# Optimization experiments

Hardware: AMD Instinct MI355X
Metric: run time of the kernel (lower is better)

## Reference

```python
import jax, jax.numpy as jnp
import numpy as np

N = 10            # n_wires
DIM = 1 << N      # 1024 state dimension
HID = 64          # number of Pauli-string observables
B, T = 4, 512

_CNOT = jnp.array([[1, 0, 0, 0], [0, 1, 0, 0], [0, 0, 0, 1], [0, 0, 1, 0]], dtype=jnp.complex64)
# 0:I 1:X 2:Y 3:Z
_PAULIS = jnp.array([[[1, 0], [0, 1]],
                     [[0, 1], [1, 0]],
                     [[0, -1j], [1j, 0]],
                     [[1, 0], [0, -1]]], dtype=jnp.complex64)

def _rx(t):
    c = jnp.cos(t / 2).astype(jnp.complex64)
    s = jnp.sin(t / 2).astype(jnp.complex64)
    return jnp.stack([jnp.stack([c, -1j * s]), jnp.stack([-1j * s, c])])

def _ry(t):
    c = jnp.cos(t / 2).astype(jnp.complex64)
    s = jnp.sin(t / 2).astype(jnp.complex64)
    return jnp.stack([jnp.stack([c, -s]), jnp.stack([s, c])])

def _apply(U, gate, qubits):
    # U <- expand_operator(gate, qubits, N) @ U, without materializing the expansion.
    # Row index bits: qubit 0 is the most significant bit (matches expand_operator).
    m = len(qubits)
    Tn = U.reshape((2,) * N + (DIM,))
    Tn = jnp.moveaxis(Tn, qubits, tuple(range(m)))
    Tn = (gate @ Tn.reshape(1 << m, -1)).reshape((2,) * N + (DIM,))
    Tn = jnp.moveaxis(Tn, tuple(range(m)), qubits)
    return Tn.reshape(DIM, DIM)

def _build_U(rx0, ry0, ry1):
    U = jnp.eye(DIM, dtype=jnp.complex64)
    for j in range(N):
        U = _apply(U, _rx(rx0[j]), (j,))
        U = _apply(U, _ry(ry0[j]), (j,))
    for j in range(N):
        U = _apply(U, _CNOT, (j, (j + 1) % N))  # control j, target (j+1)%N
    for j in range(N):
        U = _apply(U, _ry(ry1[j]), (j,))
    return U

def _build_obs(op_codes):
    # O[h] = kron of Paulis along the wire axis (qubit 0 leftmost / most significant).
    mats = _PAULIS[op_codes]  # (H, N, 2, 2)
    O = jnp.ones((op_codes.shape[0], 1, 1), jnp.complex64)
    for q in range(N):
        d = O.shape[-1]
        O = jnp.einsum('hij,hkl->hikjl', O, mats[:, q]).reshape(-1, 2 * d, 2 * d)
    return O  # (H, DIM, DIM)

def setup_inputs() -> dict:
    key = jax.random.key(0)
    ks = jax.random.split(key, 5)
    pi = 3.14159265
    return {
        'x': jax.random.normal(ks[0], (B, T, DIM), jnp.float32),
        'rx0': jax.random.uniform(ks[1], (N,), jnp.float32, -pi, pi),
        'ry0': jax.random.uniform(ks[2], (N,), jnp.float32, -pi, pi),
        'ry1': jax.random.uniform(ks[3], (N,), jnp.float32, -pi, pi),
        'op_codes': jax.random.randint(ks[4], (HID, N), 0, 4),
    }

def reference(x, rx0, ry0, ry1, op_codes):
    U = _build_U(rx0, ry0, ry1)
    O = _build_obs(op_codes)
    b, t, c = x.shape
    xf = x.reshape(b * t, c)
    # AmplitudeEncoder: L2-normalize each row into a complex state vector.
    psi = (xf / jnp.linalg.norm(xf, axis=-1, keepdims=True)).astype(jnp.complex64)
    # <psi| U^dag O U |psi> = <phi| O |phi> with phi = U psi  (same math as obs_primes)
    phi = psi @ U.T  # (BT, DIM)
    exps = jnp.einsum('bd,odk,bk->bo', phi.conj(), O, phi).real
    return exps.reshape(b, t, -1).astype(jnp.float32)
```

## Files before the change

kernel.cpp:

```cpp
#include <hip/hip_runtime.h>
#include <math.h>

#define NQ 10
#define DIM 1024
#define HID 64
#define NT 256

template<int CTRL>
__device__ __forceinline__ float fdpp(float v) {
    return __int_as_float(__builtin_amdgcn_update_dpp(
        0, __float_as_int(v), CTRL, 0xF, 0xF, true));
}

__device__ __forceinline__ void l1pair(float4 g, float& r0, float& i0, float& r1, float& i1) {
    float n0r = g.x * r0 - g.y * i0 - g.z * r1 + g.w * i1;
    float n0i = g.x * i0 + g.y * r0 - g.z * i1 - g.w * r1;
    float n1r = g.z * r0 + g.w * i0 + g.x * r1 + g.y * i1;
    float n1i = g.z * i0 - g.w * r0 + g.x * i1 - g.y * r1;
    r0 = n0r; i0 = n0i; r1 = n1r; i1 = n1i;
}
__device__ __forceinline__ void l2pair(float2 g, float& r0, float& i0, float& r1, float& i1) {
    float n0r = g.x * r0 - g.y * r1, n0i = g.x * i0 - g.y * i1;
    float n1r = g.y * r0 + g.x * r1, n1i = g.y * i0 + g.x * i1;
    r0 = n0r; i0 = n0i; r1 = n1r; i1 = n1i;
}

template<int P>
__device__ __forceinline__ float xl(float v) {
    if constexpr (P == 0)      return fdpp<0xB1>(v);
    else if constexpr (P == 1) return fdpp<0x4E>(v);
    else                       return __shfl_xor(v, 1 << P, 64);
}

template<int P>
__device__ __forceinline__ void gate4_l1(float4 g, int tid, float (&vr)[4], float (&vi)[4]) {
    const float fsb = ((tid >> P) & 1) ? 1.f : -1.f;
    const float Bs = fsb * g.y, Cs = fsb * g.z;
    #pragma unroll
    for (int m = 0; m < 4; m++) {
        float ur = xl<P>(vr[m]);
        float ui = xl<P>(vi[m]);
        float nr = g.x * vr[m] + Bs * vi[m] + Cs * ur + g.w * ui;
        float ni = g.x * vi[m] - Bs * vr[m] + Cs * ui - g.w * ur;
        vr[m] = nr; vi[m] = ni;
    }
}
template<int P>
__device__ __forceinline__ void gate4_l2(float2 g, int tid, float (&vr)[4], float (&vi)[4]) {
    const float fsb = ((tid >> P) & 1) ? 1.f : -1.f;
    const float ssf = fsb * g.y;
    #pragma unroll
    for (int m = 0; m < 4; m++) {
        float ur = xl<P>(vr[m]);
        float ui = xl<P>(vi[m]);
        vr[m] = g.x * vr[m] + ssf * ur;
        vi[m] = g.x * vi[m] + ssf * ui;
    }
}

template<int PASS, int HB, int CM>
__device__ __forceinline__ float obs_halved_p(const float (&vr)[8], const float (&vi)[8],
                                              const char* stb, int base_cx, int w1) {
    float a0 = 0.f, a1 = 0.f;
    if constexpr (HB == 3) {
        if constexpr (PASS == 1) return 0.f;
        #pragma unroll
        for (int j = 0; j < 8; j++) {
            const int r = j;
            const float2 c = *(const float2*)(stb + (base_cx ^ (r << 9)));
            float t;
            if constexpr (CM) t = vr[j] * c.y - vi[j] * c.x;
            else              t = vr[j] * c.x + vi[j] * c.y;
            const int cf = 0x40000000 | (((w1 >> r) & 1) << 31);
            if (j & 1) a1 = fmaf(__int_as_float(cf), t, a1);
            else       a0 = fmaf(__int_as_float(cf), t, a0);
        }
    } else {
        #pragma unroll
        for (int ii = 0; ii < 4; ii++) {
            const int idx = PASS * 4 + ii;
            const int r   = ((idx >> HB) << (HB + 1)) | (idx & ((1 << HB) - 1));
            const int j   = r - PASS * 8;
            const float2 c = *(const float2*)(stb + (base_cx ^ (r << 9)));
            float t;
            if constexpr (CM) t = vr[j] * c.y - vi[j] * c.x;
            else              t = vr[j] * c.x + vi[j] * c.y;
            const int cf = 0x40000000 | (((w1 >> r) & 1) << 31);
            if (ii & 1) a1 = fmaf(__int_as_float(cf), t, a1);
            else        a0 = fmaf(__int_as_float(cf), t, a0);
        }
    }
    return a0 + a1;
}
template<int PASS, int CM>
__device__ __forceinline__ float obs_full_p(const float (&vr)[8], const float (&vi)[8],
                                            const char* stb, int base_c, int w1) {
    float a0 = 0.f, a1 = 0.f;
    #pragma unroll
    for (int j = 0; j < 8; j++) {
        const int r = PASS * 8 + j;
        const float2 c = *(const float2*)(stb + base_c + (r << 9));
        float t;
        if constexpr (CM) t = vr[j] * c.y - vi[j] * c.x;
        else              t = vr[j] * c.x + vi[j] * c.y;
        const int cf = 0x3F800000 | (((w1 >> r) & 1) << 31);
        if (j & 1) a1 = fmaf(__int_as_float(cf), t, a1);
        else       a0 = fmaf(__int_as_float(cf), t, a0);
    }
    return a0 + a1;
}
template<int PASS>
__device__ __forceinline__ float obs_diag_p(const float (&vr)[8], const float (&vi)[8], int w1) {
    float a0 = 0.f, a1 = 0.f;
    #pragma unroll
    for (int j = 0; j < 8; j++) {
        const int r = PASS * 8 + j;
        float t = fmaf(vr[j], vr[j], vi[j] * vi[j]);
        const int cf = 0x3F800000 | (((w1 >> r) & 1) << 31);
        if (j & 1) a1 = fmaf(__int_as_float(cf), t, a1);
        else       a0 = fmaf(__int_as_float(cf), t, a0);
    }
    return a0 + a1;
}
__device__ __forceinline__ int4 make_meta(const int* op_codes, int o) {
    int xm = 0, yzm = 0, ny = 0;
    #pragma unroll
    for (int q = 0; q < NQ; q++) {
        int code = op_codes[o * NQ + q];
        int bit  = 1 << (NQ - 1 - q);
        if (code == 1) xm |= bit;
        else if (code == 2) { xm |= bit; yzm |= bit; ny++; }
        else if (code == 3) yzm |= bit;
    }
    const int cm = ny & 1, gflip = (ny >> 1) & 1;
    const int yh = yzm >> 6;
    int w1 = 0;
    #pragma unroll
    for (int r = 0; r < 16; r++)
        w1 |= ((__popc(r & yh) & 1) ^ gflip) << r;
    const int xmr = (xm >> 6) & 15;
    int hbc;
    if (xm == 0)      hbc = 5;
    else if (xmr)     hbc = __ffs(xmr) - 1;
    else              hbc = 4;
    return make_int4(xm, yzm & 63, w1, hbc | (cm << 3));
}
template<int PASS>
__device__ __forceinline__ float obs_one_p(int4 mt, int lane,
        const float (&vr)[8], const float (&vi)[8], const char* stb) {
    const int xm   = __builtin_amdgcn_readfirstlane(mt.x);
    const int yzml = __builtin_amdgcn_readfirstlane(mt.y);
    const int w1   = __builtin_amdgcn_readfirstlane(mt.z);
    const int knd  = __builtin_amdgcn_readfirstlane(mt.w);
    const int hbc = knd & 7, cm = knd >> 3;
    float p;
    if (hbc == 5) {
        p = obs_diag_p<PASS>(vr, vi, w1);
    } else {
        const int xml = xm & 63, xmr = (xm >> 6) & 15;
        const int base_cx = (xmr << 9) | ((lane ^ xml) << 3);
        switch (hbc | (cm << 3)) {
            case 0:     p = obs_halved_p<PASS,0,0>(vr, vi, stb, base_cx, w1); break;
            case 1:     p = obs_halved_p<PASS,1,0>(vr, vi, stb, base_cx, w1); break;
            case 2:     p = obs_halved_p<PASS,2,0>(vr, vi, stb, base_cx, w1); break;
            case 3:     p = obs_halved_p<PASS,3,0>(vr, vi, stb, base_cx, w1); break;
            case 4:     p = obs_full_p<PASS,0>(vr, vi, stb, base_cx, w1);     break;
            case 8 | 0: p = obs_halved_p<PASS,0,1>(vr, vi, stb, base_cx, w1); break;
            case 8 | 1: p = obs_halved_p<PASS,1,1>(vr, vi, stb, base_cx, w1); break;
            case 8 | 2: p = obs_halved_p<PASS,2,1>(vr, vi, stb, base_cx, w1); break;
            case 8 | 3: p = obs_halved_p<PASS,3,1>(vr, vi, stb, base_cx, w1); break;
            default:    p = obs_full_p<PASS,1>(vr, vi, stb, base_cx, w1);     break;
        }
    }
    const int sl = __popc(lane & yzml) & 1;
    return __int_as_float(__float_as_int(p) ^ (sl << 31));
}

__global__ __launch_bounds__(NT, 6) void qsa_kernel(
    const float* __restrict__ x,
    const float* __restrict__ rx0,
    const float* __restrict__ ry0,
    const float* __restrict__ ry1,
    const int*   __restrict__ op_codes,
    float* __restrict__ out)
{
    __shared__ float2 st[DIM];
    __shared__ float  cb[4][64 * 17];
    __shared__ float4 s_l1[NQ];
    __shared__ float2 s_l2[NQ];
    __shared__ int4   s_meta[HID];
    __shared__ float  wsum[4];

    const int tid  = threadIdx.x;
    const int lane = tid & 63;
    const int wave = tid >> 6;
    const int row  = blockIdx.x;

    if (tid < NQ) {
        float a = 0.5f * rx0[tid], b = 0.5f * ry0[tid];
        float c1 = cosf(a), s1 = sinf(a), c2 = cosf(b), s2 = sinf(b);
        s_l1[tid] = make_float4(c1 * c2, s1 * s2, s2 * c1, c2 * s1);
    } else if (tid < 2 * NQ) {
        float a = 0.5f * ry1[tid - NQ];
        s_l2[tid - NQ] = make_float2(cosf(a), sinf(a));
    }
    if (tid >= 64 && tid < 64 + HID)
        s_meta[tid - 64] = make_meta(op_codes, tid - 64);

    float vr[4], vi[4];
    float ssq = 0.f;
    const float* xr = x + (size_t)row * DIM;
    #pragma unroll
    for (int m = 0; m < 4; m++) {
        vr[m] = xr[tid + NT * m];
        vi[m] = 0.f;
        ssq += vr[m] * vr[m];
    }
    #pragma unroll
    for (int off = 32; off; off >>= 1) ssq += __shfl_xor(ssq, off, 64);
    if (lane == 0) wsum[wave] = ssq;
    __syncthreads();
    {
        float inv = 1.0f / sqrtf(wsum[0] + wsum[1] + wsum[2] + wsum[3]);
        #pragma unroll
        for (int m = 0; m < 4; m++) vr[m] *= inv;
    }

    {
        float4 g0 = s_l1[0];
        l1pair(g0, vr[0], vi[0], vr[2], vi[2]);
        l1pair(g0, vr[1], vi[1], vr[3], vi[3]);
        float4 g1 = s_l1[1];
        l1pair(g1, vr[0], vi[0], vr[1], vi[1]);
        l1pair(g1, vr[2], vi[2], vr[3], vi[3]);
    }
    #pragma unroll
    for (int m = 0; m < 4; m++) st[tid + NT * m] = make_float2(vr[m], vi[m]);
    __syncthreads();
    {
        int base = lane | (wave << 8);
        float2 w00 = st[base], w01 = st[base | 64], w10 = st[base | 128], w11 = st[base | 192];
        float4 g2 = s_l1[2], g3 = s_l1[3];
        l1pair(g2, w00.x, w00.y, w10.x, w10.y);
        l1pair(g2, w01.x, w01.y, w11.x, w11.y);
        l1pair(g3, w00.x, w00.y, w01.x, w01.y);
        l1pair(g3, w10.x, w10.y, w11.x, w11.y);
        st[base] = w00; st[base | 64] = w01; st[base | 128] = w10; st[base | 192] = w11;
    }
    __syncthreads();
    #pragma unroll
    for (int m = 0; m < 4; m++) { float2 t = st[tid + NT * m]; vr[m] = t.x; vi[m] = t.y; }
    gate4_l1<5>(s_l1[4], tid, vr, vi);
    gate4_l1<4>(s_l1[5], tid, vr, vi);
    gate4_l1<3>(s_l1[6], tid, vr, vi);
    gate4_l1<2>(s_l1[7], tid, vr, vi);
    gate4_l1<1>(s_l1[8], tid, vr, vi);
    gate4_l1<0>(s_l1[9], tid, vr, vi);

    #pragma unroll
    for (int m = 0; m < 4; m++) st[tid + NT * m] = make_float2(vr[m], vi[m]);
    __syncthreads();
    #pragma unroll
    for (int m = 0; m < 4; m++) {
        int d = tid + NT * m;
        int src = (d ^ (d >> 1)) ^ ((d & 1) * 0x300);
        float2 t = st[src];
        vr[m] = t.x; vi[m] = t.y;
    }
    __syncthreads();

    {
        float2 g0 = s_l2[0];
        l2pair(g0, vr[0], vi[0], vr[2], vi[2]);
        l2pair(g0, vr[1], vi[1], vr[3], vi[3]);
        float2 g1 = s_l2[1];
        l2pair(g1, vr[0], vi[0], vr[1], vi[1]);
        l2pair(g1, vr[2], vi[2], vr[3], vi[3]);
    }
    #pragma unroll
    for (int m = 0; m < 4; m++) st[tid + NT * m] = make_float2(vr[m], vi[m]);
    __syncthreads();
    {
        int base = lane | (wave << 8);
        float2 w00 = st[base], w01 = st[base | 64], w10 = st[base | 128], w11 = st[base | 192];
        float2 g2 = s_l2[2], g3 = s_l2[3];
        l2pair(g2, w00.x, w00.y, w10.x, w10.y);
        l2pair(g2, w01.x, w01.y, w11.x, w11.y);
        l2pair(g3, w00.x, w00.y, w01.x, w01.y);
        l2pair(g3, w10.x, w10.y, w11.x, w11.y);
        st[base] = w00; st[base | 64] = w01; st[base | 128] = w10; st[base | 192] = w11;
    }
    __syncthreads();
    #pragma unroll
    for (int m = 0; m < 4; m++) { float2 t = st[tid + NT * m]; vr[m] = t.x; vi[m] = t.y; }
    gate4_l2<5>(s_l2[4], tid, vr, vi);
    gate4_l2<4>(s_l2[5], tid, vr, vi);
    gate4_l2<3>(s_l2[6], tid, vr, vi);
    gate4_l2<2>(s_l2[7], tid, vr, vi);
    gate4_l2<1>(s_l2[8], tid, vr, vi);
    gate4_l2<0>(s_l2[9], tid, vr, vi);
    #pragma unroll
    for (int m = 0; m < 4; m++) st[tid + NT * m] = make_float2(vr[m], vi[m]);
    __syncthreads();

    const char* stb = (const char*)st;
    float* cbw = &cb[wave][lane * 17];
    const float* cbr = &cb[wave][(lane >> 4) * (16 * 17) + (lane & 15)];
    {
        float vra[8], via[8];
        #pragma unroll
        for (int j = 0; j < 8; j++) {
            float2 t = st[(j << 6) | lane];
            vra[j] = t.x; via[j] = t.y;
        }
        #pragma unroll 2
        for (int oo = 0; oo < 16; oo++)
            cbw[oo] = obs_one_p<0>(s_meta[(wave << 4) + oo], lane, vra, via, stb);
        #pragma unroll
        for (int j = 0; j < 8; j++) {
            float2 t = st[((8 + j) << 6) | lane];
            vra[j] = t.x; via[j] = t.y;
        }
        #pragma unroll 2
        for (int oo = 0; oo < 16; oo++)
            cbw[oo] += obs_one_p<1>(s_meta[(wave << 4) + oo], lane, vra, via, stb);
    }
    float s0 = 0.f, s1 = 0.f, s2 = 0.f, s3 = 0.f;
    #pragma unroll
    for (int k = 0; k < 16; k += 4) {
        s0 += cbr[(k + 0) * 17];
        s1 += cbr[(k + 1) * 17];
        s2 += cbr[(k + 2) * 17];
        s3 += cbr[(k + 3) * 17];
    }
    float tot = (s0 + s1) + (s2 + s3);
    tot += __shfl_xor(tot, 16, 64);
    tot += __shfl_xor(tot, 32, 64);
    if (lane < 16)
        out[(size_t)row * HID + (wave << 4) + lane] = tot;
}

extern "C" void kernel_launch(void* const* d_in, const int* in_sizes, int n_in,
                              void* d_out, int out_size, void* d_ws, size_t ws_size,
                              hipStream_t stream) {
    const float* x   = (const float*)d_in[0];
    const float* rx0 = (const float*)d_in[1];
    const float* ry0 = (const float*)d_in[2];
    const float* ry1 = (const float*)d_in[3];
    const int*   op  = (const int*)d_in[4];
    float* o = (float*)d_out;
    const int rows = in_sizes[0] / DIM;
    qsa_kernel<<<rows, NT, 0, stream>>>(x, rx0, ry0, ry1, op, o);
}
```

Before: 39.11 us.

## Process two state rows per block, sharing gate and observable metadata

Each block now simulates two input rows together, storing their complex amplitudes interleaved as float4 in shared memory. Gate coefficients, observable metadata, branch decisions and the shared-memory coefficient reads are amortized across both rows. The observable reduction is split into two chunks of eight to bound register use, and launch bounds drop from 6 to 4 waves per SIMD. The cost is higher register and LDS pressure, and half as many blocks, which lowers occupancy and parallelism.

New measurement: 70.41 us. 80.0% more time.

```diff
diff --git a/kernel.cpp b/kernel.cpp
--- a/kernel.cpp
+++ b/kernel.cpp
@@ -59,21 +59,23 @@
 }
 
 template<int PASS, int HB, int CM>
-__device__ __forceinline__ float obs_halved_p(const float (&vr)[8], const float (&vi)[8],
-                                              const char* stb, int base_cx, int w1) {
-    float a0 = 0.f, a1 = 0.f;
+__device__ __forceinline__ float2 obs_halved_p2(
+        const float (&a0r)[8], const float (&a0i)[8],
+        const float (&a1r)[8], const float (&a1i)[8],
+        const char* stb, int base_cx, int w1) {
+    float p0 = 0.f, p1 = 0.f;
     if constexpr (HB == 3) {
-        if constexpr (PASS == 1) return 0.f;
+        if constexpr (PASS == 1) return make_float2(0.f, 0.f);
         #pragma unroll
         for (int j = 0; j < 8; j++) {
-            const int r = j;
-            const float2 c = *(const float2*)(stb + (base_cx ^ (r << 9)));
-            float t;
-            if constexpr (CM) t = vr[j] * c.y - vi[j] * c.x;
-            else              t = vr[j] * c.x + vi[j] * c.y;
-            const int cf = 0x40000000 | (((w1 >> r) & 1) << 31);
-            if (j & 1) a1 = fmaf(__int_as_float(cf), t, a1);
-            else       a0 = fmaf(__int_as_float(cf), t, a0);
+            const float4 c = *(const float4*)(stb + (base_cx ^ (j << 10)));
+            float t0, t1;
+            if constexpr (CM) { t0 = a0r[j] * c.y - a0i[j] * c.x;
+                                t1 = a1r[j] * c.w - a1i[j] * c.z; }
+            else              { t0 = a0r[j] * c.x + a0i[j] * c.y;
+                                t1 = a1r[j] * c.z + a1i[j] * c.w; }
+            const float cf = __int_as_float(0x40000000 | (((w1 >> j) & 1) << 31));
+            p0 = fmaf(cf, t0, p0); p1 = fmaf(cf, t1, p1);
         }
     } else {
         #pragma unroll
@@ -81,46 +83,52 @@
             const int idx = PASS * 4 + ii;
             const int r   = ((idx >> HB) << (HB + 1)) | (idx & ((1 << HB) - 1));
             const int j   = r - PASS * 8;
-            const float2 c = *(const float2*)(stb + (base_cx ^ (r << 9)));
-            float t;
-            if constexpr (CM) t = vr[j] * c.y - vi[j] * c.x;
-            else              t = vr[j] * c.x + vi[j] * c.y;
-            const int cf = 0x40000000 | (((w1 >> r) & 1) << 31);
-            if (ii & 1) a1 = fmaf(__int_as_float(cf), t, a1);
-            else        a0 = fmaf(__int_as_float(cf), t, a0);
-        }
-    }
-    return a0 + a1;
+            const float4 c = *(const float4*)(stb + (base_cx ^ (r << 10)));
+            float t0, t1;
+            if constexpr (CM) { t0 = a0r[j] * c.y - a0i[j] * c.x;
+                                t1 = a1r[j] * c.w - a1i[j] * c.z; }
+            else              { t0 = a0r[j] * c.x + a0i[j] * c.y;
+                                t1 = a1r[j] * c.z + a1i[j] * c.w; }
+            const float cf = __int_as_float(0x40000000 | (((w1 >> r) & 1) << 31));
+            p0 = fmaf(cf, t0, p0); p1 = fmaf(cf, t1, p1);
+        }
+    }
+    return make_float2(p0, p1);
 }
 template<int PASS, int CM>
-__device__ __forceinline__ float obs_full_p(const float (&vr)[8], const float (&vi)[8],
-                                            const char* stb, int base_c, int w1) {
-    float a0 = 0.f, a1 = 0.f;
+__device__ __forceinline__ float2 obs_full_p2(
+        const float (&a0r)[8], const float (&a0i)[8],
+        const float (&a1r)[8], const float (&a1i)[8],
+        const char* stb, int base_c, int w1) {
+    float p0 = 0.f, p1 = 0.f;
     #pragma unroll
     for (int j = 0; j < 8; j++) {
         const int r = PASS * 8 + j;
-        const float2 c = *(const float2*)(stb + base_c + (r << 9));
-        float t;
-        if constexpr (CM) t = vr[j] * c.y - vi[j] * c.x;
-        else              t = vr[j] * c.x + vi[j] * c.y;
-        const int cf = 0x3F800000 | (((w1 >> r) & 1) << 31);
-        if (j & 1) a1 = fmaf(__int_as_float(cf), t, a1);
-        else       a0 = fmaf(__int_as_float(cf), t, a0);
-    }
-    return a0 + a1;
+        const float4 c = *(const float4*)(stb + (base_c ^ (r << 10)));
+        float t0, t1;
+        if constexpr (CM) { t0 = a0r[j] * c.y - a0i[j] * c.x;
+                            t1 = a1r[j] * c.w - a1i[j] * c.z; }
+        else              { t0 = a0r[j] * c.x + a0i[j] * c.y;
+                            t1 = a1r[j] * c.z + a1i[j] * c.w; }
+        const float cf = __int_as_float(0x3F800000 | (((w1 >> r) & 1) << 31));
+        p0 = fmaf(cf, t0, p0); p1 = fmaf(cf, t1, p1);
+    }
+    return make_float2(p0, p1);
 }
 template<int PASS>
-__device__ __forceinline__ float obs_diag_p(const float (&vr)[8], const float (&vi)[8], int w1) {
-    float a0 = 0.f, a1 = 0.f;
+__device__ __forceinline__ float2 obs_diag_p2(
+        const float (&a0r)[8], const float (&a0i)[8],
+        const float (&a1r)[8], const float (&a1i)[8], int w1) {
+    float p0 = 0.f, p1 = 0.f;
     #pragma unroll
     for (int j = 0; j < 8; j++) {
         const int r = PASS * 8 + j;
-        float t = fmaf(vr[j], vr[j], vi[j] * vi[j]);
-        const int cf = 0x3F800000 | (((w1 >> r) & 1) << 31);
-        if (j & 1) a1 = fmaf(__int_as_float(cf), t, a1);
-        else       a0 = fmaf(__int_as_float(cf), t, a0);
-    }
-    return a0 + a1;
+        float t0 = fmaf(a0r[j], a0r[j], a0i[j] * a0i[j]);
+        float t1 = fmaf(a1r[j], a1r[j], a1i[j] * a1i[j]);
+        const float cf = __int_as_float(0x3F800000 | (((w1 >> r) & 1) << 31));
+        p0 = fmaf(cf, t0, p0); p1 = fmaf(cf, t1, p1);
+    }
+    return make_float2(p0, p1);
 }
 __device__ __forceinline__ int4 make_meta(const int* op_codes, int o) {
     int xm = 0, yzm = 0, ny = 0;
@@ -146,37 +154,40 @@
     return make_int4(xm, yzm & 63, w1, hbc | (cm << 3));
 }
 template<int PASS>
-__device__ __forceinline__ float obs_one_p(int4 mt, int lane,
-        const float (&vr)[8], const float (&vi)[8], const char* stb) {
+__device__ __forceinline__ float2 obs_one_p2(int4 mt, int lane,
+        const float (&a0r)[8], const float (&a0i)[8],
+        const float (&a1r)[8], const float (&a1i)[8], const char* stb) {
     const int xm   = __builtin_amdgcn_readfirstlane(mt.x);
     const int yzml = __builtin_amdgcn_readfirstlane(mt.y);
     const int w1   = __builtin_amdgcn_readfirstlane(mt.z);
     const int knd  = __builtin_amdgcn_readfirstlane(mt.w);
     const int hbc = knd & 7, cm = knd >> 3;
-    float p;
+    float2 p;
     if (hbc == 5) {
-        p = obs_diag_p<PASS>(vr, vi, w1);
+        p = obs_diag_p2<PASS>(a0r, a0i, a1r, a1i, w1);
     } else {
         const int xml = xm & 63, xmr = (xm >> 6) & 15;
-        const int base_cx = (xmr << 9) | ((lane ^ xml) << 3);
+        const int base_cx = (xmr << 10) | ((lane ^ xml) << 4);
         switch (hbc | (cm << 3)) {
-            case 0:     p = obs_halved_p<PASS,0,0>(vr, vi, stb, base_cx, w1); break;
-            case 1:     p = obs_halved_p<PASS,1,0>(vr, vi, stb, base_cx, w1); break;
-            case 2:     p = obs_halved_p<PASS,2,0>(vr, vi, stb, base_cx, w1); break;
-            case 3:     p = obs_halved_p<PASS,3,0>(vr, vi, stb, base_cx, w1); break;
-            case 4:     p = obs_full_p<PASS,0>(vr, vi, stb, base_cx, w1);     break;
-            case 8 | 0: p = obs_halved_p<PASS,0,1>(vr, vi, stb, base_cx, w1); break;
-            case 8 | 1: p = obs_halved_p<PASS,1,1>(vr, vi, stb, base_cx, w1); break;
-            case 8 | 2: p = obs_halved_p<PASS,2,1>(vr, vi, stb, base_cx, w1); break;
-            case 8 | 3: p = obs_halved_p<PASS,3,1>(vr, vi, stb, base_cx, w1); break;
-            default:    p = obs_full_p<PASS,1>(vr, vi, stb, base_cx, w1);     break;
-        }
-    }
-    const int sl = __popc(lane & yzml) & 1;
-    return __int_as_float(__float_as_int(p) ^ (sl << 31));
-}
-
-__global__ __launch_bounds__(NT, 6) void qsa_kernel(
+            case 0:     p = obs_halved_p2<PASS,0,0>(a0r,a0i,a1r,a1i, stb, base_cx, w1); break;
+            case 1:     p = obs_halved_p2<PASS,1,0>(a0r,a0i,a1r,a1i, stb, base_cx, w1); break;
+            case 2:     p = obs_halved_p2<PASS,2,0>(a0r,a0i,a1r,a1i, stb, base_cx, w1); break;
+            case 3:     p = obs_halved_p2<PASS,3,0>(a0r,a0i,a1r,a1i, stb, base_cx, w1); break;
+            case 4:     p = obs_full_p2<PASS,0>(a0r,a0i,a1r,a1i, stb, base_cx, w1);     break;
+            case 8 | 0: p = obs_halved_p2<PASS,0,1>(a0r,a0i,a1r,a1i, stb, base_cx, w1); break;
+            case 8 | 1: p = obs_halved_p2<PASS,1,1>(a0r,a0i,a1r,a1i, stb, base_cx, w1); break;
+            case 8 | 2: p = obs_halved_p2<PASS,2,1>(a0r,a0i,a1r,a1i, stb, base_cx, w1); break;
+            case 8 | 3: p = obs_halved_p2<PASS,3,1>(a0r,a0i,a1r,a1i, stb, base_cx, w1); break;
+            default:    p = obs_full_p2<PASS,1>(a0r,a0i,a1r,a1i, stb, base_cx, w1);     break;
+        }
+    }
+    const int slb = (__popc(lane & yzml) & 1) << 31;
+    p.x = __int_as_float(__float_as_int(p.x) ^ slb);
+    p.y = __int_as_float(__float_as_int(p.y) ^ slb);
+    return p;
+}
+
+__global__ __launch_bounds__(NT, 4) void qsa_kernel(
     const float* __restrict__ x,
     const float* __restrict__ rx0,
     const float* __restrict__ ry0,
@@ -184,17 +195,18 @@
     const int*   __restrict__ op_codes,
     float* __restrict__ out)
 {
-    __shared__ float2 st[DIM];
-    __shared__ float  cb[4][64 * 17];
+    __shared__ float4 st4[DIM];
+    __shared__ float2 cb[4][64 * 9];
     __shared__ float4 s_l1[NQ];
     __shared__ float2 s_l2[NQ];
     __shared__ int4   s_meta[HID];
-    __shared__ float  wsum[4];
+    __shared__ float2 wsum[4];
 
     const int tid  = threadIdx.x;
     const int lane = tid & 63;
     const int wave = tid >> 6;
-    const int row  = blockIdx.x;
+    const int row0 = blockIdx.x * 2;
+    const int row1 = row0 + 1;
 
     if (tid < NQ) {
         float a = 0.5f * rx0[tid], b = 0.5f * ry0[tid];
@@ -207,137 +219,164 @@
     if (tid >= 64 && tid < 64 + HID)
         s_meta[tid - 64] = make_meta(op_codes, tid - 64);
 
-    float vr[4], vi[4];
-    float ssq = 0.f;
-    const float* xr = x + (size_t)row * DIM;
-    #pragma unroll
-    for (int m = 0; m < 4; m++) {
-        vr[m] = xr[tid + NT * m];
-        vi[m] = 0.f;
-        ssq += vr[m] * vr[m];
-    }
-    #pragma unroll
-    for (int off = 32; off; off >>= 1) ssq += __shfl_xor(ssq, off, 64);
-    if (lane == 0) wsum[wave] = ssq;
-    __syncthreads();
-    {
-        float inv = 1.0f / sqrtf(wsum[0] + wsum[1] + wsum[2] + wsum[3]);
-        #pragma unroll
-        for (int m = 0; m < 4; m++) vr[m] *= inv;
+    float vrx[4], vix[4], vry[4], viy[4];
+    {
+        const float* xp = x + (size_t)row0 * DIM;
+        float s0 = 0.f, s1 = 0.f;
+        #pragma unroll
+        for (int m = 0; m < 4; m++) {
+            vrx[m] = xp[tid + NT * m];
+            vry[m] = xp[DIM + tid + NT * m];
+            vix[m] = 0.f; viy[m] = 0.f;
+            s0 += vrx[m] * vrx[m];
+            s1 += vry[m] * vry[m];
+        }
+        #pragma unroll
+        for (int off = 32; off; off >>= 1) {
+            s0 += __shfl_xor(s0, off, 64);
+            s1 += __shfl_xor(s1, off, 64);
+        }
+        if (lane == 0) wsum[wave] = make_float2(s0, s1);
+    }
+    __syncthreads();
+    {
+        float t0 = wsum[0].x + wsum[1].x + wsum[2].x + wsum[3].x;
+        float t1 = wsum[0].y + wsum[1].y + wsum[2].y + wsum[3].y;
+        float inv0 = 1.0f / sqrtf(t0);
+        float inv1 = 1.0f / sqrtf(t1);
+        #pragma unroll
+        for (int m = 0; m < 4; m++) { vrx[m] *= inv0; vry[m] *= inv1; }
     }
 
     {
         float4 g0 = s_l1[0];
-        l1pair(g0, vr[0], vi[0], vr[2], vi[2]);
-        l1pair(g0, vr[1], vi[1], vr[3], vi[3]);
+        l1pair(g0, vrx[0], vix[0], vrx[2], vix[2]);
+        l1pair(g0, vrx[1], vix[1], vrx[3], vix[3]);
+        l1pair(g0, vry[0], viy[0], vry[2], viy[2]);
+        l1pair(g0, vry[1], viy[1], vry[3], viy[3]);
         float4 g1 = s_l1[1];
-        l1pair(g1, vr[0], vi[0], vr[1], vi[1]);
-        l1pair(g1, vr[2], vi[2], vr[3], vi[3]);
-    }
-    #pragma unroll
-    for (int m = 0; m < 4; m++) st[tid + NT * m] = make_float2(vr[m], vi[m]);
+        l1pair(g1, vrx[0], vix[0], vrx[1], vix[1]);
+        l1pair(g1, vrx[2], vix[2], vrx[3], vix[3]);
+        l1pair(g1, vry[0], viy[0], vry[1], viy[1]);
+        l1pair(g1, vry[2], viy[2], vry[3], viy[3]);
+    }
+    gate4_l1<5>(s_l1[4], tid, vrx, vix); gate4_l1<5>(s_l1[4], tid, vry, viy);
+    gate4_l1<4>(s_l1[5], tid, vrx, vix); gate4_l1<4>(s_l1[5], tid, vry, viy);
+    gate4_l1<3>(s_l1[6], tid, vrx, vix); gate4_l1<3>(s_l1[6], tid, vry, viy);
+    gate4_l1<2>(s_l1[7], tid, vrx, vix); gate4_l1<2>(s_l1[7], tid, vry, viy);
+    gate4_l1<1>(s_l1[8], tid, vrx, vix); gate4_l1<1>(s_l1[8], tid, vry, viy);
+    gate4_l1<0>(s_l1[9], tid, vrx, vix); gate4_l1<0>(s_l1[9], tid, vry, viy);
+    #pragma unroll
+    for (int m = 0; m < 4; m++)
+        st4[tid + NT * m] = make_float4(vrx[m], vix[m], vry[m], viy[m]);
     __syncthreads();
     {
         int base = lane | (wave << 8);
-        float2 w00 = st[base], w01 = st[base | 64], w10 = st[base | 128], w11 = st[base | 192];
+        float4 w00 = st4[base], w01 = st4[base | 64], w10 = st4[base | 128], w11 = st4[base | 192];
         float4 g2 = s_l1[2], g3 = s_l1[3];
         l1pair(g2, w00.x, w00.y, w10.x, w10.y);
+        l1pair(g2, w00.z, w00.w, w10.z, w10.w);
         l1pair(g2, w01.x, w01.y, w11.x, w11.y);
+        l1pair(g2, w01.z, w01.w, w11.z, w11.w);
         l1pair(g3, w00.x, w00.y, w01.x, w01.y);
+        l1pair(g3, w00.z, w00.w, w01.z, w01.w);
         l1pair(g3, w10.x, w10.y, w11.x, w11.y);
-        st[base] = w00; st[base | 64] = w01; st[base | 128] = w10; st[base | 192] = w11;
-    }
-    __syncthreads();
-    #pragma unroll
-    for (int m = 0; m < 4; m++) { float2 t = st[tid + NT * m]; vr[m] = t.x; vi[m] = t.y; }
-    gate4_l1<5>(s_l1[4], tid, vr, vi);
-    gate4_l1<4>(s_l1[5], tid, vr, vi);
-    gate4_l1<3>(s_l1[6], tid, vr, vi);
-    gate4_l1<2>(s_l1[7], tid, vr, vi);
-    gate4_l1<1>(s_l1[8], tid, vr, vi);
-    gate4_l1<0>(s_l1[9], tid, vr, vi);
-
-    #pragma unroll
-    for (int m = 0; m < 4; m++) st[tid + NT * m] = make_float2(vr[m], vi[m]);
-    __syncthreads();
+        l1pair(g3, w10.z, w10.w, w11.z, w11.w);
+        st4[base] = w00; st4[base | 64] = w01; st4[base | 128] = w10; st4[base | 192] = w11;
+    }
+    __syncthreads();
+
     #pragma unroll
     for (int m = 0; m < 4; m++) {
         int d = tid + NT * m;
         int src = (d ^ (d >> 1)) ^ ((d & 1) * 0x300);
-        float2 t = st[src];
-        vr[m] = t.x; vi[m] = t.y;
+        float4 t = st4[src];
+        vrx[m] = t.x; vix[m] = t.y; vry[m] = t.z; viy[m] = t.w;
     }
     __syncthreads();
 
     {
         float2 g0 = s_l2[0];
-        l2pair(g0, vr[0], vi[0], vr[2], vi[2]);
-        l2pair(g0, vr[1], vi[1], vr[3], vi[3]);
+        l2pair(g0, vrx[0], vix[0], vrx[2], vix[2]);
+        l2pair(g0, vrx[1], vix[1], vrx[3], vix[3]);
+        l2pair(g0, vry[0], viy[0], vry[2], viy[2]);
+        l2pair(g0, vry[1], viy[1], vry[3], viy[3]);
         float2 g1 = s_l2[1];
-        l2pair(g1, vr[0], vi[0], vr[1], vi[1]);
-        l2pair(g1, vr[2], vi[2], vr[3], vi[3]);
-    }
-    #pragma unroll
-    for (int m = 0; m < 4; m++) st[tid + NT * m] = make_float2(vr[m], vi[m]);
+        l2pair(g1, vrx[0], vix[0], vrx[1], vix[1]);
+        l2pair(g1, vrx[2], vix[2], vrx[3], vix[3]);
+        l2pair(g1, vry[0], viy[0], vry[1], viy[1]);
+        l2pair(g1, vry[2], viy[2], vry[3], viy[3]);
+    }
+    gate4_l2<5>(s_l2[4], tid, vrx, vix); gate4_l2<5>(s_l2[4], tid, vry, viy);
+    gate4_l2<4>(s_l2[5], tid, vrx, vix); gate4_l2<4>(s_l2[5], tid, vry, viy);
+    gate4_l2<3>(s_l2[6], tid, vrx, vix); gate4_l2<3>(s_l2[6], tid, vry, viy);
+    gate4_l2<2>(s_l2[7], tid, vrx, vix); gate4_l2<2>(s_l2[7], tid, vry, viy);
+    gate4_l2<1>(s_l2[8], tid, vrx, vix); gate4_l2<1>(s_l2[8], tid, vry, viy);
+    gate4_l2<0>(s_l2[9], tid, vrx, vix); gate4_l2<0>(s_l2[9], tid, vry, viy);
+    #pragma unroll
+    for (int m = 0; m < 4; m++)
+        st4[tid + NT * m] = make_float4(vrx[m], vix[m], vry[m], viy[m]);
     __syncthreads();
     {
         int base = lane | (wave << 8);
-        float2 w00 = st[base], w01 = st[base | 64], w10 = st[base | 128], w11 = st[base | 192];
+        float4 w00 = st4[base], w01 = st4[base | 64], w10 = st4[base | 128], w11 = st4[base | 192];
         float2 g2 = s_l2[2], g3 = s_l2[3];
         l2pair(g2, w00.x, w00.y, w10.x, w10.y);
+        l2pair(g2, w00.z, w00.w, w10.z, w10.w);
         l2pair(g2, w01.x, w01.y, w11.x, w11.y);
+        l2pair(g2, w01.z, w01.w, w11.z, w11.w);
         l2pair(g3, w00.x, w00.y, w01.x, w01.y);
+        l2pair(g3, w00.z, w00.w, w01.z, w01.w);
         l2pair(g3, w10.x, w10.y, w11.x, w11.y);
-        st[base] = w00; st[base | 64] = w01; st[base | 128] = w10; st[base | 192] = w11;
-    }
-    __syncthreads();
-    #pragma unroll
-    for (int m = 0; m < 4; m++) { float2 t = st[tid + NT * m]; vr[m] = t.x; vi[m] = t.y; }
-    gate4_l2<5>(s_l2[4], tid, vr, vi);
-    gate4_l2<4>(s_l2[5], tid, vr, vi);
-    gate4_l2<3>(s_l2[6], tid, vr, vi);
-    gate4_l2<2>(s_l2[7], tid, vr, vi);
-    gate4_l2<1>(s_l2[8], tid, vr, vi);
-    gate4_l2<0>(s_l2[9], tid, vr, vi);
-    #pragma unroll
-    for (int m = 0; m < 4; m++) st[tid + NT * m] = make_float2(vr[m], vi[m]);
-    __syncthreads();
-
-    const char* stb = (const char*)st;
-    float* cbw = &cb[wave][lane * 17];
-    const float* cbr = &cb[wave][(lane >> 4) * (16 * 17) + (lane & 15)];
-    {
-        float vra[8], via[8];
+        l2pair(g3, w10.z, w10.w, w11.z, w11.w);
+        st4[base] = w00; st4[base | 64] = w01; st4[base | 128] = w10; st4[base | 192] = w11;
+    }
+    __syncthreads();
+
+    const char* stb = (const char*)st4;
+    float2* cbw = &cb[wave][lane * 9];
+    const float2* cbr = &cb[wave][(lane >> 3) * (8 * 9) + (lane & 7)];
+    float a0r[8], a0i[8], a1r[8], a1i[8];
+    #pragma unroll 1
+    for (int c = 0; c < 2; c++) {
+        float2 pacc[8];
         #pragma unroll
         for (int j = 0; j < 8; j++) {
-            float2 t = st[(j << 6) | lane];
-            vra[j] = t.x; via[j] = t.y;
+            float4 t = st4[(j << 6) | lane];
+            a0r[j] = t.x; a0i[j] = t.y; a1r[j] = t.z; a1i[j] = t.w;
         }
         #pragma unroll 2
-        for (int oo = 0; oo < 16; oo++)
-            cbw[oo] = obs_one_p<0>(s_meta[(wave << 4) + oo], lane, vra, via, stb);
+        for (int j = 0; j < 8; j++)
+            pacc[j] = obs_one_p2<0>(s_meta[(wave << 4) + c * 8 + j], lane,
+                                    a0r, a0i, a1r, a1i, stb);
         #pragma unroll
         for (int j = 0; j < 8; j++) {
-            float2 t = st[((8 + j) << 6) | lane];
-            vra[j] = t.x; via[j] = t.y;
+            float4 t = st4[((8 + j) << 6) | lane];
+            a0r[j] = t.x; a0i[j] = t.y; a1r[j] = t.z; a1i[j] = t.w;
         }
         #pragma unroll 2
-        for (int oo = 0; oo < 16; oo++)
-            cbw[oo] += obs_one_p<1>(s_meta[(wave << 4) + oo], lane, vra, via, stb);
-    }
-    float s0 = 0.f, s1 = 0.f, s2 = 0.f, s3 = 0.f;
-    #pragma unroll
-    for (int k = 0; k < 16; k += 4) {
-        s0 += cbr[(k + 0) * 17];
-        s1 += cbr[(k + 1) * 17];
-        s2 += cbr[(k + 2) * 17];
-        s3 += cbr[(k + 3) * 17];
-    }
-    float tot = (s0 + s1) + (s2 + s3);
-    tot += __shfl_xor(tot, 16, 64);
-    tot += __shfl_xor(tot, 32, 64);
-    if (lane < 16)
-        out[(size_t)row * HID + (wave << 4) + lane] = tot;
+        for (int j = 0; j < 8; j++) {
+            float2 p = obs_one_p2<1>(s_meta[(wave << 4) + c * 8 + j], lane,
+                                     a0r, a0i, a1r, a1i, stb);
+            pacc[j].x += p.x; pacc[j].y += p.y;
+        }
+        #pragma unroll
+        for (int j = 0; j < 8; j++) cbw[j] = pacc[j];
+        float sx = 0.f, sy = 0.f;
+        #pragma unroll
+        for (int k = 0; k < 8; k++) {
+            float2 v = cbr[k * 9];
+            sx += v.x; sy += v.y;
+        }
+        sx += __shfl_xor(sx, 8, 64);  sy += __shfl_xor(sy, 8, 64);
+        sx += __shfl_xor(sx, 16, 64); sy += __shfl_xor(sy, 16, 64);
+        sx += __shfl_xor(sx, 32, 64); sy += __shfl_xor(sy, 32, 64);
+        if (lane < 8) {
+            const int oidx = (wave << 4) + c * 8 + lane;
+            out[(size_t)row0 * HID + oidx] = sx;
+            out[(size_t)row1 * HID + oidx] = sy;
+        }
+    }
 }
 
 extern "C" void kernel_launch(void* const* d_in, const int* in_sizes, int n_in,
@@ -350,5 +389,5 @@
     const int*   op  = (const int*)d_in[4];
     float* o = (float*)d_out;
     const int rows = in_sizes[0] / DIM;
-    qsa_kernel<<<rows, NT, 0, stream>>>(x, rx0, ry0, ry1, op, o);
-}
+    qsa_kernel<<<rows / 2, NT, 0, stream>>>(x, rx0, ry0, ry1, op, o);
+}
```
